# Performance work log

Hardware: AMD Instinct MI355X
Metric: run time of the kernel (lower is better)

## Reference

```python
import jax, jax.numpy as jnp
import numpy as np

B, R, C, E, H = 2, 16, 512, 1024, 16
D = E // H  # head_dim = 64


def setup_inputs() -> dict:
    key = jax.random.key(0)
    ks = jax.random.split(key, 9)
    s = 1.0 / np.sqrt(E)
    return {
        "x": jax.random.normal(ks[0], (B, R, C, E), dtype=jnp.float32),
        "wq": jax.random.uniform(ks[1], (E, E), jnp.float32, -s, s),
        "bq": jax.random.uniform(ks[2], (E,), jnp.float32, -s, s),
        "wk": jax.random.uniform(ks[3], (E, E), jnp.float32, -s, s),
        "bk": jax.random.uniform(ks[4], (E,), jnp.float32, -s, s),
        "wv": jax.random.uniform(ks[5], (E, E), jnp.float32, -s, s),
        "bv": jax.random.uniform(ks[6], (E,), jnp.float32, -s, s),
        "wo": jax.random.uniform(ks[7], (E, E), jnp.float32, -s, s),
        "bo": jax.random.uniform(ks[8], (E,), jnp.float32, -s, s),
    }


def reference(x, wq, bq, wk, bk, wv, bv, wo, bo):
    b, r, c, e = x.shape
    # projections: [b,r,c,e] -> [b,r,h,c,d]
    def split_heads(t):
        return t.reshape(b, r, c, H, D).transpose(0, 1, 3, 2, 4)
    q = split_heads(x @ wq + bq)
    k = split_heads(x @ wk + bk)
    v = split_heads(x @ wv + bv)
    scale = 1.0 / jnp.sqrt(jnp.asarray(D, x.dtype))
    logits = jnp.einsum('brhqd,brhkd->brhqk', q, k) * scale
    probs = jax.nn.softmax(logits, axis=-1)
    ctx = jnp.einsum('brhqk,brhkd->brhqd', probs, v)
    ctx = ctx.transpose(0, 1, 3, 2, 4).reshape(b, r, c, e)
    return ctx @ wo + bo
```

## Files before the change

kernel.cpp:

```cpp
#include <hip/hip_runtime.h>
#include <hip/hip_bf16.h>
#include <hip/hip_fp16.h>
#include <math.h>

typedef _Float16 half8 __attribute__((ext_vector_type(8)));
typedef __attribute__((ext_vector_type(4))) float floatx4;

constexpr int Bc = 2, Rc = 16, Cc = 512, Ec = 1024, Hc = 16, Dc = 64;
constexpr int Mtok = Bc * Rc * Cc;
#define QSCALE 0.180336880111120425f

__device__ inline void gl_lds16(const void* g, void* l) {
  __builtin_amdgcn_global_load_lds(
      (const __attribute__((address_space(1))) void*)g,
      (__attribute__((address_space(3))) void*)l, 16, 0, 0);
}
__device__ inline unsigned short f2h(float f) {
  __half h = __float2half_rn(f);
  return *(unsigned short*)&h;
}
__device__ inline unsigned int pack_h2(float lo, float hi) {
  __half2 p = __float22half2_rn(make_float2(lo, hi));
  return *(unsigned int*)&p;
}

__global__ __launch_bounds__(256) void cvt_x(const float* __restrict__ x,
                                             unsigned short* __restrict__ xh) {
  const size_t base = ((size_t)blockIdx.x * 256 + threadIdx.x) * 8;
  float4 a = *(const float4*)(x + base);
  float4 b = *(const float4*)(x + base + 4);
  uint4 o;
  o.x = pack_h2(a.x, a.y);
  o.y = pack_h2(a.z, a.w);
  o.z = pack_h2(b.x, b.y);
  o.w = pack_h2(b.z, b.w);
  *(uint4*)(xh + base) = o;
}

__global__ __launch_bounds__(256) void wprep(
    const float* __restrict__ w0, const float* __restrict__ w1,
    const float* __restrict__ w2, const float* __restrict__ w3,
    unsigned short* __restrict__ t0, unsigned short* __restrict__ t1,
    unsigned short* __restrict__ t2, unsigned short* __restrict__ t3) {
  __shared__ float tile[64][65];
  const int z = blockIdx.z;
  const float* W = (z == 0) ? w0 : (z == 1) ? w1 : (z == 2) ? w2 : w3;
  unsigned short* T = (z == 0) ? t0 : (z == 1) ? t1 : (z == 2) ? t2 : t3;
  const int tid = threadIdx.x;
  const int bk = blockIdx.x * 64, bn = blockIdx.y * 64;
#pragma unroll
  for (int p = 0; p < 16; ++p) {
    int idx = p * 256 + tid;
    int lk = idx >> 6, ln = idx & 63;
    tile[ln][lk] = W[(size_t)(bk + lk) * 1024 + bn + ln];
  }
  __syncthreads();
#pragma unroll
  for (int p = 0; p < 16; ++p) {
    int idx = p * 256 + tid;
    int ln = idx >> 6, lk = idx & 63;
    T[(size_t)(bn + ln) * 1024 + bk + lk] = f2h(tile[ln][lk]);
  }
}

__global__ __launch_bounds__(256, 2) void gemm_qkv(
    const unsigned short* __restrict__ xh, const unsigned short* __restrict__ wqh,
    const unsigned short* __restrict__ wkh, const unsigned short* __restrict__ wvh,
    const float* __restrict__ bq, const float* __restrict__ bk,
    const float* __restrict__ bv, unsigned short* __restrict__ qout,
    unsigned short* __restrict__ kout, unsigned short* __restrict__ vout) {
  __shared__ unsigned short As[128 * 32];
  __shared__ unsigned short Bs[256 * 32];
  const int z = blockIdx.z;
  const unsigned short* Bp = (z == 0) ? wqh : (z == 1) ? wkh : wvh;
  const float* bias = (z == 0) ? bq : (z == 1) ? bk : bv;
  const int tid = threadIdx.x;
  const int wv_ = tid >> 6, ln = tid & 63;
  const int bn = blockIdx.x * 256, bm = blockIdx.y * 128;
  floatx4 acc[4][8];
#pragma unroll
  for (int i = 0; i < 4; ++i)
#pragma unroll
    for (int j = 0; j < 8; ++j) acc[i][j] = (floatx4)(0.f);

  const int wm = (wv_ >> 1) * 64, wn = (wv_ & 1) * 128;
  const int lr = ln & 15, quad = ln >> 4;
  const int fsl = ((quad ^ ((lr >> 1) & 3)) << 3);
  const int coff = (((ln & 3) ^ ((ln >> 3) & 3)) << 3);

  for (int t = 0; t < 32; ++t) {
    const int kk = t << 5;
#pragma unroll
    for (int is = 0; is < 2; ++is) {
      const int r0 = is * 64 + wv_ * 16;
      const int row = r0 + (ln >> 2);
      gl_lds16(xh + (size_t)(bm + row) * 1024 + kk + coff, As + r0 * 32);
    }
#pragma unroll
    for (int p = 0; p < 4; ++p) {
      const int r0 = p * 64 + wv_ * 16;
      const int row = r0 + (ln >> 2);
      gl_lds16(Bp + (size_t)(bn + row) * 1024 + kk + coff, Bs + r0 * 32);
    }
    __syncthreads();
    half8 af[4], bfr[8];
#pragma unroll
    for (int i = 0; i < 4; ++i)
      af[i] = *(const half8*)&As[(wm + i * 16 + lr) * 32 + fsl];
#pragma unroll
    for (int j = 0; j < 8; ++j)
      bfr[j] = *(const half8*)&Bs[(wn + j * 16 + lr) * 32 + fsl];
#pragma unroll
    for (int i = 0; i < 4; ++i)
#pragma unroll
      for (int j = 0; j < 8; ++j)
        acc[i][j] = __builtin_amdgcn_mfma_f32_16x16x32_f16(af[i], bfr[j],
                                                           acc[i][j], 0, 0, 0);
    __syncthreads();
  }

  const int q4 = quad * 4;
  const bool odd = ln & 1;
#pragma unroll
  for (int i = 0; i < 4; ++i) {
#pragma unroll
    for (int j = 0; j < 8; ++j) {
      const int col = bn + wn + j * 16 + lr;
      float v[4];
#pragma unroll
      for (int r = 0; r < 4; ++r) v[r] = acc[i][j][r] + bias[col];
      const int m0 = bm + wm + i * 16 + q4;
      const int h = col >> 6, d = col & 63;
      const int br = m0 >> 9, c0 = m0 & 511;
      const size_t hb = ((size_t)br * 16 + h) * 32768;
      if (z == 2) {
        uint2 o;
        o.x = pack_h2(v[0], v[1]);
        o.y = pack_h2(v[2], v[3]);
        *(uint2*)(vout + hb + (size_t)d * 512 + c0) = o;
      } else {
        unsigned short* outp = (z == 0) ? qout : kout;
        if (z == 0) {
#pragma unroll
          for (int r = 0; r < 4; ++r) v[r] *= QSCALE;
        }
#pragma unroll
        for (int rp = 0; rp < 2; ++rp) {
          float a = v[2 * rp], b = v[2 * rp + 1];
          float ax = __shfl_xor(a, 1), bx = __shfl_xor(b, 1);
          unsigned int u = odd ? pack_h2(bx, b) : pack_h2(a, ax);
          const int c = c0 + 2 * rp + (odd ? 1 : 0);
          const int dd = d & ~1;
          *(unsigned int*)(outp + hb + (size_t)c * 64 + dd) = u;
        }
      }
    }
  }
}

__global__ __launch_bounds__(256, 2) void gemm_out(
    const unsigned short* __restrict__ Ah, const unsigned short* __restrict__ Bh,
    const float* __restrict__ bias, float* __restrict__ Out) {
  __shared__ unsigned short As[128 * 32];
  __shared__ unsigned short Bs[256 * 32];
  const int tid = threadIdx.x;
  const int wv_ = tid >> 6, ln = tid & 63;
  const int bn = blockIdx.x * 256, bm = blockIdx.y * 128;
  floatx4 acc[4][8];
#pragma unroll
  for (int i = 0; i < 4; ++i)
#pragma unroll
    for (int j = 0; j < 8; ++j) acc[i][j] = (floatx4)(0.f);

  const int wm = (wv_ >> 1) * 64, wn = (wv_ & 1) * 128;
  const int lr = ln & 15, quad = ln >> 4;
  const int fsl = ((quad ^ ((lr >> 1) & 3)) << 3);
  const int coff = (((ln & 3) ^ ((ln >> 3) & 3)) << 3);

  for (int t = 0; t < 32; ++t) {
    const int kk = t << 5;
#pragma unroll
    for (int is = 0; is < 2; ++is) {
      const int r0 = is * 64 + wv_ * 16;
      const int row = r0 + (ln >> 2);
      gl_lds16(Ah + (size_t)(bm + row) * 1024 + kk + coff, As + r0 * 32);
    }
#pragma unroll
    for (int p = 0; p < 4; ++p) {
      const int r0 = p * 64 + wv_ * 16;
      const int row = r0 + (ln >> 2);
      gl_lds16(Bh + (size_t)(bn + row) * 1024 + kk + coff, Bs + r0 * 32);
    }
    __syncthreads();
    half8 af[4], bfr[8];
#pragma unroll
    for (int i = 0; i < 4; ++i)
      af[i] = *(const half8*)&As[(wm + i * 16 + lr) * 32 + fsl];
#pragma unroll
    for (int j = 0; j < 8; ++j)
      bfr[j] = *(const half8*)&Bs[(wn + j * 16 + lr) * 32 + fsl];
#pragma unroll
    for (int i = 0; i < 4; ++i)
#pragma unroll
      for (int j = 0; j < 8; ++j)
        acc[i][j] = __builtin_amdgcn_mfma_f32_16x16x32_f16(af[i], bfr[j],
                                                           acc[i][j], 0, 0, 0);
    __syncthreads();
  }

  const int q4 = (ln >> 4) * 4;
#pragma unroll
  for (int i = 0; i < 4; ++i)
#pragma unroll
    for (int j = 0; j < 8; ++j)
#pragma unroll
      for (int r = 0; r < 4; ++r) {
        const int m = bm + wm + i * 16 + q4 + r;
        const int col = bn + wn + j * 16 + lr;
        Out[(size_t)m * 1024 + col] = acc[i][j][r] + bias[col];
      }
}

__global__ __launch_bounds__(256, 2) void attn_mfma(
    const unsigned short* __restrict__ Qh, const unsigned short* __restrict__ Kb,
    const unsigned short* __restrict__ Vt, unsigned short* __restrict__ Ctx) {
  __shared__ unsigned short Ks[128 * 64];
  __shared__ unsigned short Vs[64 * 128];
  __shared__ unsigned short Ps[128][136];

  const int t = threadIdx.x;
  const int w = t >> 6, ln = t & 63;
  const int lane15 = ln & 15, quad = ln >> 4;
  const bool odd = ln & 1;
  const int bh = blockIdx.x >> 2;
  const int qb = (blockIdx.x & 3) * 128;

  half8 qf[2][2];
  {
    const size_t qbase =
        ((size_t)bh * 512 + qb + w * 32 + lane15) * 64 + quad * 8;
#pragma unroll
    for (int i = 0; i < 2; ++i)
#pragma unroll
      for (int c = 0; c < 2; ++c)
        qf[i][c] = *(const half8*)(Qh + qbase + (size_t)i * 16 * 64 + c * 32);
  }

  floatx4 oacc[2][4];
#pragma unroll
  for (int i = 0; i < 2; ++i)
#pragma unroll
    for (int dj = 0; dj < 4; ++dj) oacc[i][dj] = (floatx4)(0.f);
  float lsum[2][4];
#pragma unroll
  for (int i = 0; i < 2; ++i)
#pragma unroll
    for (int r = 0; r < 4; ++r) lsum[i][r] = 0.f;

  const unsigned short* kgb = Kb + (size_t)bh * 32768;
  const unsigned short* vgb = Vt + (size_t)bh * 32768;

  for (int kt = 0; kt < 512; kt += 128) {
    __syncthreads();
    {
      const unsigned short* kq = kgb + (size_t)kt * 64;
#pragma unroll
      for (int p = 0; p < 4; ++p) {
        const int s = p * 256 + t;
        const int kr = s >> 3, kc16 = s & 7;
        gl_lds16(kq + kr * 64 + ((kc16 ^ (kr & 7)) << 3), (char*)Ks + s * 16);
        const int vr = s >> 4, vc16 = s & 15;
        gl_lds16(vgb + vr * 512 + kt + ((vc16 ^ (vr & 15)) << 3),
                 (char*)Vs + s * 16);
      }
    }
    __syncthreads();

    floatx4 sacc[2][8];
#pragma unroll
    for (int i = 0; i < 2; ++i)
#pragma unroll
      for (int j = 0; j < 8; ++j) sacc[i][j] = (floatx4)(0.f);
#pragma unroll
    for (int j = 0; j < 8; ++j) {
      const int krow = j * 16 + lane15;
      const unsigned short* kr = Ks + krow * 64;
      half8 kf0 = *(const half8*)(kr + ((quad ^ (krow & 7)) << 3));
      half8 kf1 = *(const half8*)(kr + (((4 + quad) ^ (krow & 7)) << 3));
#pragma unroll
      for (int i = 0; i < 2; ++i) {
        sacc[i][j] = __builtin_amdgcn_mfma_f32_16x16x32_f16(qf[i][0], kf0,
                                                            sacc[i][j], 0, 0, 0);
        sacc[i][j] = __builtin_amdgcn_mfma_f32_16x16x32_f16(qf[i][1], kf1,
                                                            sacc[i][j], 0, 0, 0);
      }
    }

#pragma unroll
    for (int i = 0; i < 2; ++i) {
#pragma unroll
      for (int rp = 0; rp < 2; ++rp) {
        const int rA = rp * 2, rB = rA + 1;
        const int row = w * 32 + i * 16 + quad * 4 + rA + (odd ? 1 : 0);
        unsigned short* prow = &Ps[row][lane15 & ~1];
#pragma unroll
        for (int j = 0; j < 8; ++j) {
          const float pA = exp2f(sacc[i][j][rA]);
          const float pB = exp2f(sacc[i][j][rB]);
          lsum[i][rA] += pA;
          lsum[i][rB] += pB;
          const float an = __shfl_xor(pA, 1);
          const float bn = __shfl_xor(pB, 1);
          const float lo = odd ? bn : pA;
          const float hi = odd ? pB : an;
          *(unsigned int*)(prow + j * 16) = pack_h2(lo, hi);
        }
      }
    }

#pragma unroll
    for (int kc = 0; kc < 4; ++kc) {
      half8 pa0 = *(const half8*)&Ps[w * 32 + lane15][kc * 32 + quad * 8];
      half8 pa1 = *(const half8*)&Ps[w * 32 + 16 + lane15][kc * 32 + quad * 8];
#pragma unroll
      for (int dj = 0; dj < 4; ++dj) {
        const int drow = dj * 16 + lane15;
        half8 vf = *(const half8*)(
            Vs + drow * 128 + (((kc * 4 + quad) ^ (drow & 15)) << 3));
        oacc[0][dj] = __builtin_amdgcn_mfma_f32_16x16x32_f16(pa0, vf,
                                                             oacc[0][dj], 0, 0, 0);
        oacc[1][dj] = __builtin_amdgcn_mfma_f32_16x16x32_f16(pa1, vf,
                                                             oacc[1][dj], 0, 0, 0);
      }
    }
  }

  float invl[2][4];
#pragma unroll
  for (int i = 0; i < 2; ++i)
#pragma unroll
    for (int r = 0; r < 4; ++r) {
      float ls = lsum[i][r];
#pragma unroll
      for (int off = 1; off < 16; off <<= 1) ls += __shfl_xor(ls, off);
      invl[i][r] = 1.f / ls;
    }
  const int br = bh >> 4, h = bh & 15;
  const size_t mbase = (size_t)br * 512 + qb + w * 32;
#pragma unroll
  for (int i = 0; i < 2; ++i)
#pragma unroll
    for (int dj = 0; dj < 4; ++dj) {
      const int e = h * 64 + dj * 16 + lane15;
      const int ee = e & ~1;
#pragma unroll
      for (int rp = 0; rp < 2; ++rp) {
        const int rA = 2 * rp, rB = rA + 1;
        float a = oacc[i][dj][rA] * invl[i][rA];
        float b = oacc[i][dj][rB] * invl[i][rB];
        float ax = __shfl_xor(a, 1), bx = __shfl_xor(b, 1);
        unsigned int u = odd ? pack_h2(bx, b) : pack_h2(a, ax);
        const size_t m = mbase + i * 16 + quad * 4 + rA + (odd ? 1 : 0);
        *(unsigned int*)(Ctx + m * 1024 + ee) = u;
      }
    }
}

extern "C" void kernel_launch(void* const* d_in, const int* in_sizes, int n_in,
                              void* d_out, int out_size, void* d_ws,
                              size_t ws_size, hipStream_t stream) {
  const float* x = (const float*)d_in[0];
  const float* wq = (const float*)d_in[1];
  const float* bq = (const float*)d_in[2];
  const float* wk = (const float*)d_in[3];
  const float* bk = (const float*)d_in[4];
  const float* wv = (const float*)d_in[5];
  const float* bv = (const float*)d_in[6];
  const float* wo = (const float*)d_in[7];
  const float* bo = (const float*)d_in[8];
  float* out = (float*)d_out;

  char* w = (char*)d_ws;
  const size_t MiB = 1ull << 20;
  unsigned short* qbuf = (unsigned short*)(w + 0 * MiB);
  unsigned short* kbuf = (unsigned short*)(w + 32 * MiB);
  unsigned short* vtb = (unsigned short*)(w + 64 * MiB);
  unsigned short* xh = (unsigned short*)(w + 96 * MiB);
  unsigned short* ctx = (unsigned short*)(w + 128 * MiB);
  unsigned short* wqh = (unsigned short*)(w + 160 * MiB);
  unsigned short* wkh = (unsigned short*)(w + 162 * MiB);
  unsigned short* wvh = (unsigned short*)(w + 164 * MiB);
  unsigned short* woh = (unsigned short*)(w + 166 * MiB);

  cvt_x<<<8192, 256, 0, stream>>>(x, xh);
  wprep<<<dim3(16, 16, 4), 256, 0, stream>>>(wq, wk, wv, wo, wqh, wkh, wvh,
                                             woh);

  gemm_qkv<<<dim3(4, 128, 3), 256, 0, stream>>>(xh, wqh, wkh, wvh, bq, bk, bv,
                                                qbuf, kbuf, vtb);

  attn_mfma<<<2048, 256, 0, stream>>>(qbuf, kbuf, vtb, ctx);

  gemm_out<<<dim3(4, 128), 256, 0, stream>>>(ctx, woh, bo, out);
}
```

Baseline: 394.4 us.

## Double-buffer GEMM LDS tiles with register prefetch in QKV and output projections

Both projection GEMMs now use two LDS buffers. The next K-tile is loaded from global memory into registers while MFMAs run on the current tile, then written to the alternate LDS buffer, so one barrier per iteration replaces two and global latency overlaps compute. The direct global-to-LDS loads are replaced by ordinary vector loads plus LDS stores. This doubles LDS use and adds register pressure, which may hurt occupancy at 2 blocks per CU.

```diff
diff --git a/kernel.cpp b/kernel.cpp
--- a/kernel.cpp
+++ b/kernel.cpp
@@ -69,8 +69,8 @@
     const float* __restrict__ bq, const float* __restrict__ bk,
     const float* __restrict__ bv, unsigned short* __restrict__ qout,
     unsigned short* __restrict__ kout, unsigned short* __restrict__ vout) {
-  __shared__ unsigned short As[128 * 32];
-  __shared__ unsigned short Bs[256 * 32];
+  __shared__ unsigned short As[2 * 128 * 32];
+  __shared__ unsigned short Bs[2 * 256 * 32];
   const int z = blockIdx.z;
   const unsigned short* Bp = (z == 0) ? wqh : (z == 1) ? wkh : wvh;
   const float* bias = (z == 0) ? bq : (z == 1) ? bk : bv;
@@ -87,36 +87,66 @@
   const int lr = ln & 15, quad = ln >> 4;
   const int fsl = ((quad ^ ((lr >> 1) & 3)) << 3);
   const int coff = (((ln & 3) ^ ((ln >> 3) & 3)) << 3);
+  const int srow = ln >> 2;
+  const int slot8 = (ln & 3) << 3;
+
+  const unsigned short* aG = xh + (size_t)(bm + wv_ * 16 + srow) * 1024 + coff;
+  const unsigned short* bG = Bp + (size_t)(bn + wv_ * 16 + srow) * 1024 + coff;
+  const int lrowA = (wv_ * 16 + srow) * 32 + slot8;
+
+  uint4 ra[2], rb[4];
+#pragma unroll
+  for (int is = 0; is < 2; ++is)
+    ra[is] = *(const uint4*)(aG + (size_t)is * 64 * 1024);
+#pragma unroll
+  for (int p = 0; p < 4; ++p)
+    rb[p] = *(const uint4*)(bG + (size_t)p * 64 * 1024);
+#pragma unroll
+  for (int is = 0; is < 2; ++is)
+    *(uint4*)&As[is * 64 * 32 + lrowA] = ra[is];
+#pragma unroll
+  for (int p = 0; p < 4; ++p)
+    *(uint4*)&Bs[p * 64 * 32 + lrowA] = rb[p];
+  __syncthreads();
 
   for (int t = 0; t < 32; ++t) {
-    const int kk = t << 5;
-#pragma unroll
-    for (int is = 0; is < 2; ++is) {
-      const int r0 = is * 64 + wv_ * 16;
-      const int row = r0 + (ln >> 2);
-      gl_lds16(xh + (size_t)(bm + row) * 1024 + kk + coff, As + r0 * 32);
-    }
-#pragma unroll
-    for (int p = 0; p < 4; ++p) {
-      const int r0 = p * 64 + wv_ * 16;
-      const int row = r0 + (ln >> 2);
-      gl_lds16(Bp + (size_t)(bn + row) * 1024 + kk + coff, Bs + r0 * 32);
-    }
-    __syncthreads();
+    const int cur = t & 1;
+    if (t < 31) {
+      const int kk = (t + 1) << 5;
+#pragma unroll
+      for (int is = 0; is < 2; ++is)
+        ra[is] = *(const uint4*)(aG + (size_t)is * 64 * 1024 + kk);
+#pragma unroll
+      for (int p = 0; p < 4; ++p)
+        rb[p] = *(const uint4*)(bG + (size_t)p * 64 * 1024 + kk);
+    }
+    const unsigned short* Ab = As + cur * 128 * 32;
+    const unsigned short* Bb = Bs + cur * 256 * 32;
     half8 af[4], bfr[8];
 #pragma unroll
     for (int i = 0; i < 4; ++i)
-      af[i] = *(const half8*)&As[(wm + i * 16 + lr) * 32 + fsl];
+      af[i] = *(const half8*)&Ab[(wm + i * 16 + lr) * 32 + fsl];
 #pragma unroll
     for (int j = 0; j < 8; ++j)
-      bfr[j] = *(const half8*)&Bs[(wn + j * 16 + lr) * 32 + fsl];
+      bfr[j] = *(const half8*)&Bb[(wn + j * 16 + lr) * 32 + fsl];
 #pragma unroll
     for (int i = 0; i < 4; ++i)
 #pragma unroll
       for (int j = 0; j < 8; ++j)
         acc[i][j] = __builtin_amdgcn_mfma_f32_16x16x32_f16(af[i], bfr[j],
                                                            acc[i][j], 0, 0, 0);
-    __syncthreads();
+    if (t < 31) {
+      const int nb = cur ^ 1;
+      unsigned short* Aw = As + nb * 128 * 32;
+      unsigned short* Bw = Bs + nb * 256 * 32;
+#pragma unroll
+      for (int is = 0; is < 2; ++is)
+        *(uint4*)&Aw[is * 64 * 32 + lrowA] = ra[is];
+#pragma unroll
+      for (int p = 0; p < 4; ++p)
+        *(uint4*)&Bw[p * 64 * 32 + lrowA] = rb[p];
+      __syncthreads();
+    }
   }
 
   const int q4 = quad * 4;
@@ -161,8 +191,8 @@
 __global__ __launch_bounds__(256, 2) void gemm_out(
     const unsigned short* __restrict__ Ah, const unsigned short* __restrict__ Bh,
     const float* __restrict__ bias, float* __restrict__ Out) {
-  __shared__ unsigned short As[128 * 32];
-  __shared__ unsigned short Bs[256 * 32];
+  __shared__ unsigned short As[2 * 128 * 32];
+  __shared__ unsigned short Bs[2 * 256 * 32];
   const int tid = threadIdx.x;
   const int wv_ = tid >> 6, ln = tid & 63;
   const int bn = blockIdx.x * 256, bm = blockIdx.y * 128;
@@ -176,36 +206,66 @@
   const int lr = ln & 15, quad = ln >> 4;
   const int fsl = ((quad ^ ((lr >> 1) & 3)) << 3);
   const int coff = (((ln & 3) ^ ((ln >> 3) & 3)) << 3);
+  const int srow = ln >> 2;
+  const int slot8 = (ln & 3) << 3;
+
+  const unsigned short* aG = Ah + (size_t)(bm + wv_ * 16 + srow) * 1024 + coff;
+  const unsigned short* bG = Bh + (size_t)(bn + wv_ * 16 + srow) * 1024 + coff;
+  const int lrowA = (wv_ * 16 + srow) * 32 + slot8;
+
+  uint4 ra[2], rb[4];
+#pragma unroll
+  for (int is = 0; is < 2; ++is)
+    ra[is] = *(const uint4*)(aG + (size_t)is * 64 * 1024);
+#pragma unroll
+  for (int p = 0; p < 4; ++p)
+    rb[p] = *(const uint4*)(bG + (size_t)p * 64 * 1024);
+#pragma unroll
+  for (int is = 0; is < 2; ++is)
+    *(uint4*)&As[is * 64 * 32 + lrowA] = ra[is];
+#pragma unroll
+  for (int p = 0; p < 4; ++p)
+    *(uint4*)&Bs[p * 64 * 32 + lrowA] = rb[p];
+  __syncthreads();
 
   for (int t = 0; t < 32; ++t) {
-    const int kk = t << 5;
-#pragma unroll
-    for (int is = 0; is < 2; ++is) {
-      const int r0 = is * 64 + wv_ * 16;
-      const int row = r0 + (ln >> 2);
-      gl_lds16(Ah + (size_t)(bm + row) * 1024 + kk + coff, As + r0 * 32);
-    }
-#pragma unroll
-    for (int p = 0; p < 4; ++p) {
-      const int r0 = p * 64 + wv_ * 16;
-      const int row = r0 + (ln >> 2);
-      gl_lds16(Bh + (size_t)(bn + row) * 1024 + kk + coff, Bs + r0 * 32);
-    }
-    __syncthreads();
+    const int cur = t & 1;
+    if (t < 31) {
+      const int kk = (t + 1) << 5;
+#pragma unroll
+      for (int is = 0; is < 2; ++is)
+        ra[is] = *(const uint4*)(aG + (size_t)is * 64 * 1024 + kk);
+#pragma unroll
+      for (int p = 0; p < 4; ++p)
+        rb[p] = *(const uint4*)(bG + (size_t)p * 64 * 1024 + kk);
+    }
+    const unsigned short* Ab = As + cur * 128 * 32;
+    const unsigned short* Bb = Bs + cur * 256 * 32;
     half8 af[4], bfr[8];
 #pragma unroll
     for (int i = 0; i < 4; ++i)
-      af[i] = *(const half8*)&As[(wm + i * 16 + lr) * 32 + fsl];
+      af[i] = *(const half8*)&Ab[(wm + i * 16 + lr) * 32 + fsl];
 #pragma unroll
     for (int j = 0; j < 8; ++j)
-      bfr[j] = *(const half8*)&Bs[(wn + j * 16 + lr) * 32 + fsl];
+      bfr[j] = *(const half8*)&Bb[(wn + j * 16 + lr) * 32 + fsl];
 #pragma unroll
     for (int i = 0; i < 4; ++i)
 #pragma unroll
       for (int j = 0; j < 8; ++j)
         acc[i][j] = __builtin_amdgcn_mfma_f32_16x16x32_f16(af[i], bfr[j],
                                                            acc[i][j], 0, 0, 0);
-    __syncthreads();
+    if (t < 31) {
+      const int nb = cur ^ 1;
+      unsigned short* Aw = As + nb * 128 * 32;
+      unsigned short* Bw = Bs + nb * 256 * 32;
+#pragma unroll
+      for (int is = 0; is < 2; ++is)
+        *(uint4*)&Aw[is * 64 * 32 + lrowA] = ra[is];
+#pragma unroll
+      for (int p = 0; p < 4; ++p)
+        *(uint4*)&Bw[p * 64 * 32 + lrowA] = rb[p];
+      __syncthreads();
+    }
   }
 
   const int q4 = (ln >> 4) * 4;
```

After: 407.3 us. 1.03x slower.
